# Kernel optimization log

Measured on AMD Instinct MI355X. Metric: run time of the kernel, lower is better.

Reference implementation:

```python
import jax, jax.numpy as jnp
import numpy as np

EPS = 1e-12  # torch F.normalize clamp_min eps


def _agnn_conv(x, src, dst, beta, n):
    # x: [N, D]; src/dst: [E] (message flows src -> dst, softmax over dst's in-edges)
    xn = x / jnp.maximum(jnp.linalg.norm(x, axis=-1, keepdims=True), EPS)
    alpha = beta[0] * jnp.sum(xn[src] * xn[dst], axis=-1)            # [E] cosine sim * beta
    amax = jax.ops.segment_max(alpha, dst, num_segments=n)           # stable segment softmax
    ex = jnp.exp(alpha - amax[dst])
    denom = jax.ops.segment_sum(ex, dst, num_segments=n)
    w = ex / denom[dst]                                              # [E]
    return jax.ops.segment_sum(x[src] * w[:, None], dst, num_segments=n)


def setup_inputs() -> dict:
    key = jax.random.key(0)
    ks = jax.random.split(key, 8)
    N, E, G = 131072, 4194304, 2048
    x = jax.random.normal(ks[0], (N, 75), dtype=jnp.float32)
    edge_index = jax.random.randint(ks[1], (2, E), 0, N, dtype=jnp.int64)
    batch = jnp.sort(jax.random.randint(ks[2], (N,), 0, G, dtype=jnp.int64))
    lin1_w = jax.random.normal(ks[3], (16, 75), dtype=jnp.float32) * (1.0 / np.sqrt(75))
    lin1_b = jnp.zeros((16,), jnp.float32)
    beta1 = jnp.ones((1,), jnp.float32)   # prop1: requires_grad=False, beta=1
    beta2 = jnp.ones((1,), jnp.float32)   # prop2: learnable beta, init 1
    lin2_w = jax.random.normal(ks[4], (64, 16), dtype=jnp.float32) * (1.0 / np.sqrt(16))
    lin2_b = jnp.zeros((64,), jnp.float32)
    gather_w = jax.random.normal(ks[5], (1, 64), dtype=jnp.float32) * (1.0 / np.sqrt(64))
    gather_b = jnp.zeros((1,), jnp.float32)
    return {"x": x, "edge_index": edge_index, "batch": batch, "num_graphs": G,
            "lin1_w": lin1_w, "lin1_b": lin1_b, "beta1": beta1, "beta2": beta2,
            "lin2_w": lin2_w, "lin2_b": lin2_b, "gather_w": gather_w, "gather_b": gather_b}


def reference(x, edge_index, batch, num_graphs, lin1_w, lin1_b, beta1, beta2,
              lin2_w, lin2_b, gather_w, gather_b):
    n = x.shape[0]
    # PyG AGNNConv adds self-loops by default
    loops = jnp.arange(n, dtype=edge_index.dtype)
    src = jnp.concatenate([edge_index[0], loops])
    dst = jnp.concatenate([edge_index[1], loops])
    # dropout is identity in eval mode
    h = jax.nn.relu(x @ lin1_w.T + lin1_b)          # [N, 16]
    h = _agnn_conv(h, src, dst, beta1, n)
    h = _agnn_conv(h, src, dst, beta2, n)
    h = h @ lin2_w.T + lin2_b                        # [N, 64]
    y = jax.ops.segment_sum(h, batch, num_segments=num_graphs)  # global_add_pool [G, 64]
    return y @ gather_w.T + gather_b                 # [G, 1]
```

## Files before the change

kernel.cpp:

```cpp
#include <hip/hip_runtime.h>
#include <hip/hip_bf16.h>
#include <hip/hip_fp16.h>
#include <math.h>

#define SSEPS 1e-24f
#define NPB 256
#define NPB_SHIFT 8
#define SRC_BITS 17
#define SRC_MASK ((1 << SRC_BITS) - 1)
#define NB 512
#define CAP_B 8832
#define SC_EDGES 4096
#define SCB 512
#define MG_T 512
#define MG_LIN 4096
#define CSR_T 512
#define DBINS 256

union QRowU { int2 v; _Float16 h[4]; };


__global__ __launch_bounds__(MG_T) void mega1(
    const int* __restrict__ src, const int* __restrict__ dst, int E,
    int* __restrict__ gcnt, int* __restrict__ packed, int nScat,
    const float* __restrict__ x, const float* __restrict__ W1,
    const float* __restrict__ b1, int* __restrict__ rec1, int N, int D,
    const float* __restrict__ l2w, const float* __restrict__ l2b,
    const float* __restrict__ gw, float* __restrict__ vbuf,
    float* __restrict__ out, const float* __restrict__ gb, int G) {
    __shared__ int sh[1216];
    int bid = blockIdx.x;
    int t = threadIdx.x;

    if (bid < nScat) {
        int* h = sh;
        int* dl = sh + SCB;
        int base = bid * SC_EDGES;
        int ed[8], es[8];
        int nv = 0;
#pragma unroll
        for (int k = 0; k < 8; ++k) {
            int i = base + k * MG_T + t;
            if (i < E) {
                ed[nv] = __builtin_nontemporal_load(&dst[i]);
                es[nv] = __builtin_nontemporal_load(&src[i]);
                ++nv;
            }
        }
        h[t] = 0;
        __syncthreads();
        for (int k = 0; k < nv; ++k) atomicAdd(&h[ed[k] >> NPB_SHIFT], 1);
        __syncthreads();
        {
            int c = h[t];
            int gp = c ? atomicAdd(&gcnt[t], c) : 0;
            dl[t] = t * CAP_B + gp;
            h[t] = 0;
        }
        __syncthreads();
        for (int k = 0; k < nv; ++k) {
            int d = ed[k];
            int b = d >> NPB_SHIFT;
            int pos = atomicAdd(&h[b], 1);
            int gi = dl[b] + pos;
            if (gi < (b + 1) * CAP_B)
                packed[gi] = ((d & (NPB - 1)) << SRC_BITS) | es[k];
        }
    } else if (bid < nScat + MG_LIN) {
        float* Ws = (float*)sh;
        float* Bs = (float*)sh + 1200;
        for (int i = t; i < 16 * D; i += MG_T) Ws[i] = W1[i];
        if (t < 16) Bs[t] = b1[t];
        __syncthreads();
        int node = (bid - nScat) * (MG_T >> 4) + (t >> 4);
        int c = t & 15;
        if (node >= N) return;
        const float* xr = x + (size_t)node * D;
        float acc = Bs[c];
        for (int k = 0; k < D; ++k) acc = fmaf(xr[k], Ws[c * D + k], acc);
        float hv = fmaxf(acc, 0.f);
        float hn = __shfl_xor(hv, 1);
        if (!(c & 1)) {
            union { _Float16 hh[2]; int i; } u;
            u.hh[0] = (_Float16)hv;
            u.hh[1] = (_Float16)hn;
            rec1[8 * node + (c >> 1)] = u.i;
        }
    } else if (bid == nScat + MG_LIN) {
        if (t < 16) {
            float a = 0.f;
            for (int j = 0; j < 64; ++j) a = fmaf(gw[j], l2w[j * 16 + t], a);
            vbuf[t] = a;
        } else if (t == 16) {
            float a = 0.f;
            for (int j = 0; j < 64; ++j) a = fmaf(gw[j], l2b[j], a);
            vbuf[16] = a;
        }
    } else {
        int g = (bid - (nScat + MG_LIN + 1)) * MG_T + t;
        if (g < G) out[g] = gb[0];
    }
}

__global__ __launch_bounds__(CSR_T) void csr_build(
    const int* __restrict__ packed, const int* __restrict__ gcnt,
    int* __restrict__ deg, int* __restrict__ offs,
    int* __restrict__ csr_src, int* __restrict__ hist, int N) {
    __shared__ int ldeg[NPB];
    __shared__ int lcur[NPB];
    __shared__ int lhist[DBINS];
    __shared__ int wsum[4];
    int b = blockIdx.x;
    int t = threadIdx.x;
    int e0 = b * CAP_B;
    int cnt = gcnt[b];
    if (cnt > CAP_B) cnt = CAP_B;
    if (t < NPB) ldeg[t] = 0;
    if (t < DBINS) lhist[t] = 0;
    __syncthreads();
    for (int i = t; i < cnt; i += CSR_T)
        atomicAdd(&ldeg[packed[e0 + i] >> SRC_BITS], 1);
    __syncthreads();
    if (t < NPB) {
        int v = ldeg[t];
        atomicAdd(&lhist[v < DBINS ? v : DBINS - 1], 1);
        int lane = t & 63;
        int incl = v;
#pragma unroll
        for (int off = 1; off < 64; off <<= 1) {
            int up = __shfl_up(incl, off);
            if (lane >= off) incl += up;
        }
        if (lane == 63) wsum[t >> 6] = incl;
        lcur[t] = incl - v;
    }
    __syncthreads();
    if (t < NPB) {
        int w = t >> 6;
        int basep = 0;
        for (int k = 0; k < w; ++k) basep += wsum[k];
        int ex = lcur[t] + basep;
        int node = (b << NPB_SHIFT) + t;
        if (node < N) {
            deg[node] = ldeg[t];
            offs[node] = e0 + ex;
        }
        lcur[t] = ex;
    }
    if (t < DBINS && t >= NPB) {}
    __syncthreads();
    for (int i = t; i < cnt; i += CSR_T) {
        int p = packed[e0 + i];
        int pos = atomicAdd(&lcur[p >> SRC_BITS], 1);
        csr_src[e0 + pos] = p & SRC_MASK;
    }
    if (t < DBINS && lhist[t]) atomicAdd(&hist[t], lhist[t]);
}

__global__ void deg_scan(const int* __restrict__ hist, int* __restrict__ cursor) {
    __shared__ int s[DBINS];
    int t = threadIdx.x;
    int h = hist[t];
    s[t] = h;
    __syncthreads();
    for (int off = 1; off < DBINS; off <<= 1) {
        int a = (t >= off) ? s[t - off] : 0;
        __syncthreads();
        s[t] += a;
        __syncthreads();
    }
    cursor[t] = s[t] - h;
}

__global__ void deg_scatter(const int* __restrict__ deg, const int* __restrict__ offs,
                            int* __restrict__ cursor, int* __restrict__ perm,
                            int* __restrict__ sdeg, int* __restrict__ soffs, int N) {
    __shared__ int lh[DBINS];
    __shared__ int lb[DBINS];
    int t = threadIdx.x;
    if (t < DBINS) lh[t] = 0;
    __syncthreads();
    int i = blockIdx.x * blockDim.x + t;
    int bin = 0, r = 0, dv = 0;
    if (i < N) {
        dv = deg[i];
        bin = dv < DBINS ? dv : DBINS - 1;
        r = atomicAdd(&lh[bin], 1);
    }
    __syncthreads();
    if (t < DBINS && lh[t]) lb[t] = atomicAdd(&cursor[t], lh[t]);
    __syncthreads();
    if (i < N) {
        int p = lb[bin] + r;
        perm[p] = i;
        sdeg[p] = dv;
        soffs[p] = offs[i];
    }
}

__global__ __launch_bounds__(256) void agnn_conv1(
    const int* __restrict__ rec1,
    const int* __restrict__ soffs, const int* __restrict__ sdeg,
    const int* __restrict__ csr, const int* __restrict__ perm,
    const float* __restrict__ beta_p,
    int* __restrict__ rec2, int N) {
    int tid = blockIdx.x * blockDim.x + threadIdx.x;
    int slot = tid >> 2;
    int q = tid & 3;
    if (slot >= N) return;
    int node = perm[slot];
    float beta = beta_p[0];
    const int2* rp = (const int2*)rec1;

    QRowU rdu;
    rdu.v = rp[4 * node + q];
    float xd[4];
#pragma unroll
    for (int k = 0; k < 4; ++k) xd[k] = (float)rdu.h[k];

    float ssd = 0.f;
#pragma unroll
    for (int k = 0; k < 4; ++k) ssd = fmaf(xd[k], xd[k], ssd);
    ssd += __shfl_xor(ssd, 1);
    ssd += __shfl_xor(ssd, 2);
    float invsd = rsqrtf(fmaxf(ssd, SSEPS));

    float e0 = __expf(beta * ssd * invsd * invsd);
    float denom = e0;
    float acc[4];
#pragma unroll
    for (int k = 0; k < 4; ++k) acc[k] = e0 * xd[k];

    int start = soffs[slot], cnt = sdeg[slot];
    int i = 0;
    for (; i + 8 <= cnt; i += 8) {
        int j[8];
        QRowU r[8];
#pragma unroll
        for (int u = 0; u < 8; ++u) j[u] = __builtin_nontemporal_load(&csr[start + i + u]);
#pragma unroll
        for (int u = 0; u < 8; ++u) r[u].v = rp[4 * j[u] + q];
#pragma unroll
        for (int u = 0; u < 8; ++u) {
            float d = 0.f, ss = 0.f;
            float hs[4];
#pragma unroll
            for (int k = 0; k < 4; ++k) {
                hs[k] = (float)r[u].h[k];
                d = fmaf(xd[k], hs[k], d);
                ss = fmaf(hs[k], hs[k], ss);
            }
            d += __shfl_xor(d, 1);
            d += __shfl_xor(d, 2);
            ss += __shfl_xor(ss, 1);
            ss += __shfl_xor(ss, 2);
            float ee = __expf(beta * d * invsd * rsqrtf(fmaxf(ss, SSEPS)));
            denom += ee;
#pragma unroll
            for (int k = 0; k < 4; ++k) acc[k] = fmaf(ee, hs[k], acc[k]);
        }
    }
    for (; i < cnt; ++i) {
        int j = __builtin_nontemporal_load(&csr[start + i]);
        QRowU r;
        r.v = rp[4 * j + q];
        float d = 0.f, ss = 0.f;
        float hs[4];
#pragma unroll
        for (int k = 0; k < 4; ++k) {
            hs[k] = (float)r.h[k];
            d = fmaf(xd[k], hs[k], d);
            ss = fmaf(hs[k], hs[k], ss);
        }
        d += __shfl_xor(d, 1);
        d += __shfl_xor(d, 2);
        ss += __shfl_xor(ss, 1);
        ss += __shfl_xor(ss, 2);
        float ee = __expf(beta * d * invsd * rsqrtf(fmaxf(ss, SSEPS)));
        denom += ee;
#pragma unroll
        for (int k = 0; k < 4; ++k) acc[k] = fmaf(ee, hs[k], acc[k]);
    }

    float inv = 1.f / denom;
    QRowU w;
#pragma unroll
    for (int k = 0; k < 4; ++k) w.h[k] = (_Float16)(acc[k] * inv);
    ((int2*)rec2)[4 * node + q] = w.v;
}

__global__ __launch_bounds__(256) void agnn_conv2(
    const int* __restrict__ rec2,
    const int* __restrict__ soffs, const int* __restrict__ sdeg,
    const int* __restrict__ csr, const int* __restrict__ perm,
    const float* __restrict__ beta_p,
    const float* __restrict__ vbuf, const int* __restrict__ batch,
    float* __restrict__ out, int N) {
    int tid = blockIdx.x * blockDim.x + threadIdx.x;
    int slot = tid >> 2;
    int q = tid & 3;
    if (slot >= N) return;
    int node = perm[slot];
    float beta = beta_p[0];
    const int2* rp = (const int2*)rec2;

    float vq[4];
#pragma unroll
    for (int k = 0; k < 4; ++k) vq[k] = vbuf[4 * q + k];

    QRowU rdu;
    rdu.v = rp[4 * node + q];
    float xd[4];
#pragma unroll
    for (int k = 0; k < 4; ++k) xd[k] = (float)rdu.h[k];

    float ssd = 0.f, pd = 0.f;
#pragma unroll
    for (int k = 0; k < 4; ++k) {
        ssd = fmaf(xd[k], xd[k], ssd);
        pd = fmaf(vq[k], xd[k], pd);
    }
    ssd += __shfl_xor(ssd, 1);
    ssd += __shfl_xor(ssd, 2);
    pd += __shfl_xor(pd, 1);
    pd += __shfl_xor(pd, 2);
    float invsd = rsqrtf(fmaxf(ssd, SSEPS));

    float e0 = __expf(beta * ssd * invsd * invsd);
    float denom = e0;
    float acc = e0 * pd;

    int start = soffs[slot], cnt = sdeg[slot];
    int i = 0;
    for (; i + 8 <= cnt; i += 8) {
        int j[8];
        QRowU r[8];
#pragma unroll
        for (int u = 0; u < 8; ++u) j[u] = __builtin_nontemporal_load(&csr[start + i + u]);
#pragma unroll
        for (int u = 0; u < 8; ++u) r[u].v = rp[4 * j[u] + q];
#pragma unroll
        for (int u = 0; u < 8; ++u) {
            float d = 0.f, ss = 0.f, pv = 0.f;
#pragma unroll
            for (int k = 0; k < 4; ++k) {
                float hs = (float)r[u].h[k];
                d = fmaf(xd[k], hs, d);
                ss = fmaf(hs, hs, ss);
                pv = fmaf(vq[k], hs, pv);
            }
            d += __shfl_xor(d, 1);
            d += __shfl_xor(d, 2);
            ss += __shfl_xor(ss, 1);
            ss += __shfl_xor(ss, 2);
            pv += __shfl_xor(pv, 1);
            pv += __shfl_xor(pv, 2);
            float ee = __expf(beta * d * invsd * rsqrtf(fmaxf(ss, SSEPS)));
            denom += ee;
            acc = fmaf(ee, pv, acc);
        }
    }
    for (; i < cnt; ++i) {
        int j = __builtin_nontemporal_load(&csr[start + i]);
        QRowU r;
        r.v = rp[4 * j + q];
        float d = 0.f, ss = 0.f, pv = 0.f;
#pragma unroll
        for (int k = 0; k < 4; ++k) {
            float hs = (float)r.h[k];
            d = fmaf(xd[k], hs, d);
            ss = fmaf(hs, hs, ss);
            pv = fmaf(vq[k], hs, pv);
        }
        d += __shfl_xor(d, 1);
        d += __shfl_xor(d, 2);
        ss += __shfl_xor(ss, 1);
        ss += __shfl_xor(ss, 2);
        pv += __shfl_xor(pv, 1);
        pv += __shfl_xor(pv, 2);
        float ee = __expf(beta * d * invsd * rsqrtf(fmaxf(ss, SSEPS)));
        denom += ee;
        acc = fmaf(ee, pv, acc);
    }
    if (q == 0) atomicAdd(&out[batch[node]], acc / denom + vbuf[16]);
}


extern "C" void kernel_launch(void* const* d_in, const int* in_sizes, int n_in,
                              void* d_out, int out_size, void* d_ws, size_t ws_size,
                              hipStream_t stream) {
    const float* x = (const float*)d_in[0];
    const int* edge_index = (const int*)d_in[1];
    const int* batch = (const int*)d_in[2];
    const float* lin1_w = (const float*)d_in[4];
    const float* lin1_b = (const float*)d_in[5];
    const float* beta1 = (const float*)d_in[6];
    const float* beta2 = (const float*)d_in[7];
    const float* lin2_w = (const float*)d_in[8];
    const float* lin2_b = (const float*)d_in[9];
    const float* gather_w = (const float*)d_in[10];
    const float* gather_b = (const float*)d_in[11];
    float* out = (float*)d_out;

    const int N = in_sizes[2];
    const int E = in_sizes[1] / 2;
    const int D = in_sizes[0] / N;
    const int G = out_size;

    const int* src = edge_index;
    const int* dst = edge_index + E;

    float* w = (float*)d_ws;
    int* rec1 = (int*)w;                 w += (size_t)N * 8;
    int* rec2 = (int*)w;                 w += (size_t)N * 8;
    float* vbuf = w;                     w += 32;
    int* deg = (int*)w;                  w += N;
    int* offs = (int*)w;                 w += N;
    int* packed = (int*)w;               w += (size_t)NB * CAP_B;
    int* csr_src = (int*)w;              w += (size_t)NB * CAP_B;
    int* gcnt = (int*)w;                 w += NB;
    int* hist = (int*)w;                 w += DBINS;
    int* cursor = (int*)w;               w += DBINS;
    int* perm = (int*)w;                 w += N;
    int* sdeg = (int*)w;                 w += N;
    int* soffs = (int*)w;                w += N;

    const int B = 256;
    dim3 gridNode4((4 * N + B - 1) / B);

    hipMemsetAsync(gcnt, 0, (NB + DBINS) * sizeof(int), stream);

    int nScat = (E + SC_EDGES - 1) / SC_EDGES;
    int nLin = (N + (MG_T / 16) - 1) / (MG_T / 16);
    int nOut = (G + MG_T - 1) / MG_T;
    dim3 megaGrid(nScat + nLin + 1 + nOut);
    mega1<<<megaGrid, MG_T, 0, stream>>>(src, dst, E, gcnt, packed, nScat,
                                         x, lin1_w, lin1_b, rec1, N, D,
                                         lin2_w, lin2_b, gather_w, vbuf,
                                         out, gather_b, G);

    csr_build<<<dim3(NB), CSR_T, 0, stream>>>(packed, gcnt, deg, offs,
                                              csr_src, hist, N);

    deg_scan<<<dim3(1), DBINS, 0, stream>>>(hist, cursor);
    deg_scatter<<<dim3((N + B - 1) / B), B, 0, stream>>>(deg, offs, cursor, perm,
                                                         sdeg, soffs, N);

    agnn_conv1<<<gridNode4, B, 0, stream>>>(rec1, soffs, sdeg, csr_src, perm,
                                            beta1, rec2, N);
    agnn_conv2<<<gridNode4, B, 0, stream>>>(rec2, soffs, sdeg, csr_src, perm,
                                            beta2, vbuf, batch, out, N);
}
```

Before: 329.8 us.

## Fold degree sort into csr_build with per-block local degree bucketing

Removes the global degree histogram, scan and scatter kernels. Each csr_build block now sorts its own 256 nodes by degree (64 bins) in shared memory and writes perm/sdeg/soffs directly, so the load-balancing permutation becomes block-local instead of global. csr_build also moves to 1024 threads per block. This saves two launches and a global pass, but degree grouping across blocks is lost, which may raise load imbalance in the conv kernels.

```diff
diff --git a/kernel.cpp b/kernel.cpp
--- a/kernel.cpp
+++ b/kernel.cpp
@@ -14,8 +14,8 @@
 #define SCB 512
 #define MG_T 512
 #define MG_LIN 4096
-#define CSR_T 512
-#define DBINS 256
+#define CSR_T 1024
+#define DB 64
 
 union QRowU { int2 v; _Float16 h[4]; };
 
@@ -104,11 +104,13 @@
 
 __global__ __launch_bounds__(CSR_T) void csr_build(
     const int* __restrict__ packed, const int* __restrict__ gcnt,
-    int* __restrict__ deg, int* __restrict__ offs,
-    int* __restrict__ csr_src, int* __restrict__ hist, int N) {
+    int* __restrict__ perm, int* __restrict__ sdeg, int* __restrict__ soffs,
+    int* __restrict__ csr_src, int N) {
     __shared__ int ldeg[NPB];
     __shared__ int lcur[NPB];
-    __shared__ int lhist[DBINS];
+    __shared__ int lex[NPB];
+    __shared__ int dhist[DB];
+    __shared__ int dcur[DB];
     __shared__ int wsum[4];
     int b = blockIdx.x;
     int t = threadIdx.x;
@@ -116,14 +118,14 @@
     int cnt = gcnt[b];
     if (cnt > CAP_B) cnt = CAP_B;
     if (t < NPB) ldeg[t] = 0;
-    if (t < DBINS) lhist[t] = 0;
+    if (t < DB) dhist[t] = 0;
     __syncthreads();
     for (int i = t; i < cnt; i += CSR_T)
         atomicAdd(&ldeg[packed[e0 + i] >> SRC_BITS], 1);
     __syncthreads();
     if (t < NPB) {
         int v = ldeg[t];
-        atomicAdd(&lhist[v < DBINS ? v : DBINS - 1], 1);
+        atomicAdd(&dhist[v < DB ? v : DB - 1], 1);
         int lane = t & 63;
         int incl = v;
 #pragma unroll
@@ -140,61 +142,37 @@
         int basep = 0;
         for (int k = 0; k < w; ++k) basep += wsum[k];
         int ex = lcur[t] + basep;
-        int node = (b << NPB_SHIFT) + t;
-        if (node < N) {
-            deg[node] = ldeg[t];
-            offs[node] = e0 + ex;
-        }
+        lex[t] = ex;
         lcur[t] = ex;
     }
-    if (t < DBINS && t >= NPB) {}
     __syncthreads();
     for (int i = t; i < cnt; i += CSR_T) {
         int p = packed[e0 + i];
         int pos = atomicAdd(&lcur[p >> SRC_BITS], 1);
         csr_src[e0 + pos] = p & SRC_MASK;
     }
-    if (t < DBINS && lhist[t]) atomicAdd(&hist[t], lhist[t]);
-}
-
-__global__ void deg_scan(const int* __restrict__ hist, int* __restrict__ cursor) {
-    __shared__ int s[DBINS];
-    int t = threadIdx.x;
-    int h = hist[t];
-    s[t] = h;
+    if (t < DB) {
+        int h = dhist[t];
+        int incl = h;
+#pragma unroll
+        for (int off = 1; off < 64; off <<= 1) {
+            int up = __shfl_up(incl, off);
+            if (t >= off) incl += up;
+        }
+        dcur[t] = incl - h;
+    }
     __syncthreads();
-    for (int off = 1; off < DBINS; off <<= 1) {
-        int a = (t >= off) ? s[t - off] : 0;
-        __syncthreads();
-        s[t] += a;
-        __syncthreads();
-    }
-    cursor[t] = s[t] - h;
-}
-
-__global__ void deg_scatter(const int* __restrict__ deg, const int* __restrict__ offs,
-                            int* __restrict__ cursor, int* __restrict__ perm,
-                            int* __restrict__ sdeg, int* __restrict__ soffs, int N) {
-    __shared__ int lh[DBINS];
-    __shared__ int lb[DBINS];
-    int t = threadIdx.x;
-    if (t < DBINS) lh[t] = 0;
-    __syncthreads();
-    int i = blockIdx.x * blockDim.x + t;
-    int bin = 0, r = 0, dv = 0;
-    if (i < N) {
-        dv = deg[i];
-        bin = dv < DBINS ? dv : DBINS - 1;
-        r = atomicAdd(&lh[bin], 1);
-    }
-    __syncthreads();
-    if (t < DBINS && lh[t]) lb[t] = atomicAdd(&cursor[t], lh[t]);
-    __syncthreads();
-    if (i < N) {
-        int p = lb[bin] + r;
-        perm[p] = i;
-        sdeg[p] = dv;
-        soffs[p] = offs[i];
+    if (t < NPB) {
+        int v = ldeg[t];
+        int bin = v < DB ? v : DB - 1;
+        int p = atomicAdd(&dcur[bin], 1);
+        int slot = (b << NPB_SHIFT) + p;
+        int node = (b << NPB_SHIFT) + t;
+        if (node < N) {
+            perm[slot] = node;
+            sdeg[slot] = v;
+            soffs[slot] = e0 + lex[t];
+        }
     }
 }
 
@@ -414,13 +392,9 @@
     int* rec1 = (int*)w;                 w += (size_t)N * 8;
     int* rec2 = (int*)w;                 w += (size_t)N * 8;
     float* vbuf = w;                     w += 32;
-    int* deg = (int*)w;                  w += N;
-    int* offs = (int*)w;                 w += N;
     int* packed = (int*)w;               w += (size_t)NB * CAP_B;
     int* csr_src = (int*)w;              w += (size_t)NB * CAP_B;
     int* gcnt = (int*)w;                 w += NB;
-    int* hist = (int*)w;                 w += DBINS;
-    int* cursor = (int*)w;               w += DBINS;
     int* perm = (int*)w;                 w += N;
     int* sdeg = (int*)w;                 w += N;
     int* soffs = (int*)w;                w += N;
@@ -428,7 +402,7 @@
     const int B = 256;
     dim3 gridNode4((4 * N + B - 1) / B);
 
-    hipMemsetAsync(gcnt, 0, (NB + DBINS) * sizeof(int), stream);
+    hipMemsetAsync(gcnt, 0, NB * sizeof(int), stream);
 
     int nScat = (E + SC_EDGES - 1) / SC_EDGES;
     int nLin = (N + (MG_T / 16) - 1) / (MG_T / 16);
@@ -439,12 +413,8 @@
                                          lin2_w, lin2_b, gather_w, vbuf,
                                          out, gather_b, G);
 
-    csr_build<<<dim3(NB), CSR_T, 0, stream>>>(packed, gcnt, deg, offs,
-                                              csr_src, hist, N);
-
-    deg_scan<<<dim3(1), DBINS, 0, stream>>>(hist, cursor);
-    deg_scatter<<<dim3((N + B - 1) / B), B, 0, stream>>>(deg, offs, cursor, perm,
-                                                         sdeg, soffs, N);
+    csr_build<<<dim3(NB), CSR_T, 0, stream>>>(packed, gcnt, perm, sdeg, soffs,
+                                              csr_src, N);
 
     agnn_conv1<<<gridNode4, B, 0, stream>>>(rec1, soffs, sdeg, csr_src, perm,
                                             beta1, rec2, N);
```

After: 326.3 us. No clear change (-1.1%).
